# Performance work log

Measured on AMD Instinct MI355X. Metric: run time of the kernel, lower is better.

The kernel has to match this reference:

```python
import jax, jax.numpy as jnp
import numpy as np

B, T, I, H, HOUT = 512, 256, 32, 128, 1
H2 = H // 2


def setup_inputs() -> dict:
    key = jax.random.key(0)
    ks = jax.random.split(key, 16)
    s = lambda *shape: 1.0 / np.sqrt(H)
    def u(k, shape):
        return jax.random.uniform(k, shape, jnp.float32, -1.0 / np.sqrt(H), 1.0 / np.sqrt(H))
    return {
        "x": jax.random.normal(ks[0], (B, T, I), jnp.float32),
        # layer 0 LSTM weights (PyTorch layout: [4H, in], gate order i,f,g,o)
        "w_ih0": u(ks[1], (4 * H, I)),
        "w_hh0": u(ks[2], (4 * H, H)),
        "b_ih0": u(ks[3], (4 * H,)),
        "b_hh0": u(ks[4], (4 * H,)),
        # layer 1 LSTM weights
        "w_ih1": u(ks[5], (4 * H, H)),
        "w_hh1": u(ks[6], (4 * H, H)),
        "b_ih1": u(ks[7], (4 * H,)),
        "b_hh1": u(ks[8], (4 * H,)),
        # MLP head: Linear(H, H//2) -> ReLU -> Linear(H//2, HOUT)
        "fc1_w": u(ks[9], (H2, H)),
        "fc1_b": u(ks[10], (H2,)),
        "fc2_w": u(ks[11], (HOUT, H2)),
        "fc2_b": u(ks[12], (HOUT,)),
    }


def _lstm_layer(x, w_ih, w_hh, b_ih, b_hh):
    # x: (B, T, in) -> h sequence (B, T, H). Dropout is eval-mode identity.
    b, t, _ = x.shape
    h_dim = w_hh.shape[1]
    # precompute input-to-gate projections for the whole sequence (one big GEMM)
    xg = jnp.einsum("bti,gi->btg", x, w_ih) + b_ih + b_hh  # (B, T, 4H)
    xg = jnp.swapaxes(xg, 0, 1)  # (T, B, 4H) for scan

    def step(carry, g_t):
        h, c = carry
        gates = g_t + h @ w_hh.T  # (B, 4H)
        i, f, g, o = jnp.split(gates, 4, axis=-1)  # PyTorch gate order i,f,g,o
        i = jax.nn.sigmoid(i)
        f = jax.nn.sigmoid(f)
        g = jnp.tanh(g)
        o = jax.nn.sigmoid(o)
        c_new = f * c + i * g
        h_new = o * jnp.tanh(c_new)
        return (h_new, c_new), h_new

    zeros = jnp.zeros((b, h_dim), x.dtype)
    _, hs = jax.lax.scan(step, (zeros, zeros), xg)
    return jnp.swapaxes(hs, 0, 1)  # (B, T, H)


def reference(x, w_ih0, w_hh0, b_ih0, b_hh0, w_ih1, w_hh1, b_ih1, b_hh1,
              fc1_w, fc1_b, fc2_w, fc2_b):
    h0 = _lstm_layer(x, w_ih0, w_hh0, b_ih0, b_hh0)   # (B, T, H)
    h1 = _lstm_layer(h0, w_ih1, w_hh1, b_ih1, b_hh1)  # (B, T, H)
    last = h1[:, -1, :]  # (B, H); dropout = identity in eval
    z = jax.nn.relu(last @ fc1_w.T + fc1_b)  # (B, H//2)
    return z @ fc2_w.T + fc2_b  # (B, forecast_horizon)
```

## Files before the change

### kernel.cpp

```cpp
#include <hip/hip_runtime.h>

#define NB 512
#define NT 256
#define NI 32
#define NH 128
#define NG 512
#define WIN 4
#define NWIN 64
#define RING 16
#define NWRK 192

#define L2E  1.4426950408889634f
#define L2E2 2.8853900817779268f

typedef __attribute__((ext_vector_type(8))) short bf16x8;
typedef __attribute__((ext_vector_type(4))) float f32x4;

__device__ __forceinline__ unsigned short f2bf_rne(float f) {
    unsigned u = __float_as_uint(f);
    return (unsigned short)((u + 0x7FFFu + ((u >> 16) & 1u)) >> 16);
}
__device__ __forceinline__ void split2(float a, float b, unsigned& hi, unsigned& lo) {
    unsigned short ha = f2bf_rne(a), hb = f2bf_rne(b);
    float ra = a - __uint_as_float((unsigned)ha << 16);
    float rb = b - __uint_as_float((unsigned)hb << 16);
    hi = (unsigned)ha | ((unsigned)hb << 16);
    lo = (unsigned)f2bf_rne(ra) | ((unsigned)f2bf_rne(rb) << 16);
}
__device__ __forceinline__ bf16x8 u4bf(uint4 u) {
    union { uint4 u; bf16x8 v; } c; c.u = u; return c.v;
}
#define MFMA16(accv, av, bv) \
    accv = __builtin_amdgcn_mfma_f32_16x16x32_bf16(av, bv, accv, 0, 0, 0)

__device__ __forceinline__ void lds_barrier() {
    asm volatile("s_waitcnt lgkmcnt(0)\n\ts_barrier" ::: "memory");
}
__device__ __forceinline__ void vm_drain() {
    asm volatile("s_waitcnt vmcnt(0)" ::: "memory");
}

__device__ __forceinline__ unsigned long long ald64(const unsigned long long* p) {
    return __hip_atomic_load(p, __ATOMIC_RELAXED, __HIP_MEMORY_SCOPE_AGENT);
}
__device__ __forceinline__ void ast64(unsigned long long* p, unsigned long long v) {
    __hip_atomic_store(p, v, __ATOMIC_RELAXED, __HIP_MEMORY_SCOPE_AGENT);
}
__device__ __forceinline__ unsigned aldu(const unsigned* p) {
    return __hip_atomic_load(p, __ATOMIC_RELAXED, __HIP_MEMORY_SCOPE_AGENT);
}
__device__ __forceinline__ void astu(unsigned* p, unsigned v) {
    __hip_atomic_store(p, v, __ATOMIC_RELAXED, __HIP_MEMORY_SCOPE_AGENT);
}

__device__ __forceinline__ float activ(float mi, float mf, float mg, float mo,
                                       float& c) {
    float ei = exp2f(mi), ef = exp2f(mf), eg = exp2f(mg), eo = exp2f(mo);
    float rf  = __builtin_amdgcn_rcpf(1.0f + ef);
    float rig = __builtin_amdgcn_rcpf((1.0f + ei) * (1.0f + eg));
    float cn  = c * rf + (1.0f - eg) * rig;
    c = cn;
    float ec = exp2f(cn * -L2E2);
    float rh = __builtin_amdgcn_rcpf((1.0f + eo) * (1.0f + ec));
    return (1.0f - ec) * rh;
}

__global__ __launch_bounds__(512, 1)
void fused(const float* __restrict__ x,
           const float* __restrict__ w_hh0, const float* __restrict__ w_hh1,
           const float* __restrict__ w_ih0, const float* __restrict__ b_ih0,
           const float* __restrict__ b_hh0,
           const float* __restrict__ w_ih1, const float* __restrict__ b_ih1,
           const float* __restrict__ b_hh1,
           const float* __restrict__ fc1w, const float* __restrict__ fc1b,
           const float* __restrict__ fc2w, const float* __restrict__ fc2b,
           unsigned long long* __restrict__ h0pl,
           float* __restrict__ xgr,
           float* __restrict__ h1s, float* __restrict__ out,
           unsigned* __restrict__ ctr0, unsigned* __restrict__ flagW,
           unsigned* __restrict__ ctr1)
{
    __shared__ __align__(16) unsigned short HA[2][16][128];
    __shared__ __align__(16) unsigned short HL[2][16][128];

    const int bid  = blockIdx.x;
    const int tid  = threadIdx.x;
    const int wv   = tid >> 6;
    const int lane = tid & 63;
    const int quad = lane >> 4;
    const int ml   = lane & 15;

    if (bid >= 64) {
        const int wk = bid - 64;
        for (int tile = wk; tile < 32 * NWIN; tile += NWRK) {
            const int w  = tile >> 5;
            const int pp = tile & 31;
            while (aldu(&ctr0[pp * 16]) < (unsigned)(4 * w + 4))
                __builtin_amdgcn_s_sleep(8);
            if (w >= RING)
                while (aldu(&ctr1[pp * 16]) < (unsigned)(w - (RING - 1)))
                    __builtin_amdgcn_s_sleep(8);
            asm volatile("" ::: "memory");

            bf16x8 A[4][4][2];
#pragma unroll
            for (int tt = 0; tt < 4; ++tt)
#pragma unroll
                for (int q = 0; q < 4; ++q)
#pragma unroll
                    for (int pl = 0; pl < 2; ++pl) {
                        const unsigned long long* ap =
                            h0pl + (((size_t)(4 * w + tt) * 2 + pl) * 32 + pp) * 512
                                 + ml * 32 + q * 8 + quad * 2;
                        unsigned long long a0 = ald64(ap), a1 = ald64(ap + 1);
                        uint4 U;
                        U.x = (unsigned)a0; U.y = (unsigned)(a0 >> 32);
                        U.z = (unsigned)a1; U.w = (unsigned)(a1 >> 32);
                        A[tt][q][pl] = u4bf(U);
                    }

            f32x4 acc[4][4] = {};
#pragma unroll
            for (int nt = 0; nt < 4; ++nt) {
                const float* bw = w_ih1
                    + (size_t)(wv * 64 + nt * 16 + ml) * NH + quad * 8;
                bf16x8 bh[4], bl[4];
#pragma unroll
                for (int q = 0; q < 4; ++q) {
                    float4 v0 = *(const float4*)(bw + q * 32);
                    float4 v1 = *(const float4*)(bw + q * 32 + 4);
                    uint4 H, L;
                    split2(v0.x, v0.y, H.x, L.x); split2(v0.z, v0.w, H.y, L.y);
                    split2(v1.x, v1.y, H.z, L.z); split2(v1.z, v1.w, H.w, L.w);
                    bh[q] = u4bf(H); bl[q] = u4bf(L);
                }
#pragma unroll
                for (int tt = 0; tt < 4; ++tt)
#pragma unroll
                    for (int q = 0; q < 4; ++q) {
                        MFMA16(acc[tt][nt], A[tt][q][0], bh[q]);
                        MFMA16(acc[tt][nt], A[tt][q][1], bh[q]);
                        MFMA16(acc[tt][nt], A[tt][q][0], bl[q]);
                    }
            }

            const int slot = w & (RING - 1);
            float* cb = xgr + ((size_t)slot * 32 + pp) * WIN * 8192;
#pragma unroll
            for (int nt = 0; nt < 4; ++nt) {
                int n = wv * 64 + nt * 16 + ml;
                float s = ((n >> 7) == 2) ? L2E2 : L2E;
                float nbs = -(b_ih1[n] + b_hh1[n]) * s;
#pragma unroll
                for (int tt = 0; tt < 4; ++tt) {
                    float* cp = cb + (size_t)tt * 8192 + n * 16 + quad * 4;
                    float v0 = fmaf(acc[tt][nt][0], -s, nbs);
                    float v1 = fmaf(acc[tt][nt][1], -s, nbs);
                    float v2 = fmaf(acc[tt][nt][2], -s, nbs);
                    float v3 = fmaf(acc[tt][nt][3], -s, nbs);
                    ast64((unsigned long long*)cp,
                          (unsigned long long)__float_as_uint(v0) |
                          ((unsigned long long)__float_as_uint(v1) << 32));
                    ast64((unsigned long long*)(cp + 2),
                          (unsigned long long)__float_as_uint(v2) |
                          ((unsigned long long)__float_as_uint(v3) << 32));
                }
            }
            vm_drain();
            __syncthreads();
            if (tid == 0) astu(&flagW[pp * 64 + w], 1u);
        }
        return;
    }

    const int role = bid >> 5;
    const int p    = bid & 31;
    const int j    = 16 * wv + ml;
    const float* wsrc = role ? w_hh1 : w_hh0;

    bf16x8 wh[4][4], wl[4][4];
#pragma unroll
    for (int t = 0; t < 4; ++t) {
        const float sc = (t == 2) ? L2E2 : L2E;
#pragma unroll
        for (int q = 0; q < 4; ++q) {
            int n = (t * 8 + wv) * 16 + ml;
            const float* s = wsrc + (size_t)n * NH + q * 32 + quad * 8;
            float4 v0 = *(const float4*)s;
            float4 v1 = *(const float4*)(s + 4);
            uint4 H, L;
            split2(v0.x * sc, v0.y * sc, H.x, L.x); split2(v0.z * sc, v0.w * sc, H.y, L.y);
            split2(v1.x * sc, v1.y * sc, H.z, L.z); split2(v1.z * sc, v1.w * sc, H.w, L.w);
            wh[t][q] = u4bf(H);
            wl[t][q] = u4bf(L);
        }
    }

    int ro[4];
#pragma unroll
    for (int q = 0; q < 4; ++q)
        ro[q] = ((ml * 256 + q * 64 + quad * 16) ^ ((ml & 7) << 4));
    int wo[4];
#pragma unroll
    for (int r = 0; r < 4; ++r) {
        int m = quad * 4 + r;
        wo[r] = ((m * 256 + j * 2) ^ ((m & 7) << 4));
    }

    float cr[4] = {};
#pragma unroll
    for (int r = 0; r < 4; ++r) {
        *(unsigned short*)((char*)&HA[0][0][0] + wo[r]) = 0;
        *(unsigned short*)((char*)&HL[0][0][0] + wo[r]) = 0;
    }
    __syncthreads();

    if (role == 0) {
        bf16x8 wi_h[4], wi_l[4];
        float nb[4];
#pragma unroll
        for (int t = 0; t < 4; ++t) {
            const float sc = (t == 2) ? L2E2 : L2E;
            int n = (t * 8 + wv) * 16 + ml;
            const float* s = w_ih0 + (size_t)n * NI + quad * 8;
            float4 v0 = *(const float4*)s;
            float4 v1 = *(const float4*)(s + 4);
            uint4 H, L;
            split2(v0.x * sc, v0.y * sc, H.x, L.x); split2(v0.z * sc, v0.w * sc, H.y, L.y);
            split2(v1.x * sc, v1.y * sc, H.z, L.z); split2(v1.z * sc, v1.w * sc, H.w, L.w);
            wi_h[t] = u4bf(H);
            wi_l[t] = u4bf(L);
            int nn = t * 128 + j;
            nb[t] = -(b_ih0[nn] + b_hh0[nn]) * sc;
        }

        const int erow = tid >> 5;
        const int eoff = erow * 256 + (((tid & 31) * 8) ^ ((erow & 7) << 4));

        const float* xrow = x + (size_t)(p * 16 + ml) * NT * NI + quad * 8;
        auto xload = [&](float4& a, float4& b, int T) __attribute__((always_inline)) {
            const float* sp = xrow + (size_t)T * NI;
            a = *(const float4*)sp;
            b = *(const float4*)(sp + 4);
        };

        auto exp0 = [&](int T, int BUF) __attribute__((always_inline)) {
            unsigned long long vh =
                *(const unsigned long long*)((const char*)&HA[BUF][0][0] + eoff);
            unsigned long long vl =
                *(const unsigned long long*)((const char*)&HL[BUF][0][0] + eoff);
            ast64(h0pl + (((size_t)(T - 1) * 2 + 0) * 32 + p) * 512 + tid, vh);
            ast64(h0pl + (((size_t)(T - 1) * 2 + 1) * 32 + p) * 512 + tid, vl);
        };

        auto step0 = [&](int TL, int BUF, float4 x0, float4 x1)
            __attribute__((always_inline)) {
            const char* hb = (const char*)&HA[BUF][0][0];
            const char* lb = (const char*)&HL[BUF][0][0];
            char* hbn = (char*)&HA[BUF ^ 1][0][0];
            char* lbn = (char*)&HL[BUF ^ 1][0][0];
            uint4 XH, XL;
            split2(x0.x, x0.y, XH.x, XL.x); split2(x0.z, x0.w, XH.y, XL.y);
            split2(x1.x, x1.y, XH.z, XL.z); split2(x1.z, x1.w, XH.w, XL.w);
            bf16x8 xh = u4bf(XH), xl = u4bf(XL);
            f32x4 P[4] = {}, Q[4] = {};
#pragma unroll
            for (int t = 0; t < 4; ++t) {
                MFMA16(P[t], xh, wi_h[t]);
                MFMA16(Q[t], xl, wi_h[t]);
                MFMA16(Q[t], xh, wi_l[t]);
            }
#pragma unroll
            for (int q = 0; q < 4; ++q) {
                bf16x8 ah = *(const bf16x8*)(hb + ro[q]);
                bf16x8 al = *(const bf16x8*)(lb + ro[q]);
#pragma unroll
                for (int t = 0; t < 4; ++t) {
                    MFMA16(P[t], ah, wh[t][q]);
                    MFMA16(Q[t], al, wh[t][q]);
                    if (q & 1) { MFMA16(P[t], ah, wl[t][q]); }
                    else       { MFMA16(Q[t], ah, wl[t][q]); }
                }
            }
#pragma unroll
            for (int r = 0; r < 4; ++r) {
                float mi = nb[0] - P[0][r] - Q[0][r];
                float mf = nb[1] - P[1][r] - Q[1][r];
                float mg = nb[2] - P[2][r] - Q[2][r];
                float mo = nb[3] - P[3][r] - Q[3][r];
                float hn = activ(mi, mf, mg, mo, cr[r]);
                unsigned short hi = f2bf_rne(hn);
                float res = hn - __uint_as_float((unsigned)hi << 16);
                unsigned short lo = f2bf_rne(res);
                *(unsigned short*)(hbn + wo[r]) = hi;
                *(unsigned short*)(lbn + wo[r]) = lo;
            }
        };

        float4 xa0, xa1, xb0, xb1;
        xload(xa0, xa1, 0);
        for (int t = 0; t < 256; t += 2) {
            if (t > 0) {
                exp0(t, 0);
                if ((t & 3) == 0) {
                    vm_drain();
                    __syncthreads();
                    if (tid == 0) astu(&ctr0[p * 16], (unsigned)t);
                }
            }
            xload(xb0, xb1, t + 1);
            step0(t, 0, xa0, xa1);
            lds_barrier();
            exp0(t + 1, 1);
            xload(xa0, xa1, t + 2 > 255 ? 255 : t + 2);
            step0(t + 1, 1, xb0, xb1);
            lds_barrier();
        }
        exp0(256, 0);
        vm_drain();
        __syncthreads();
        if (tid == 0) astu(&ctr0[p * 16], 256u);
        return;
    }

    {
        auto pxg = [&](float (&d)[4][4], int u) __attribute__((always_inline)) {
            int slot = (u >> 2) & (RING - 1);
            int tt   = u & 3;
            const float* b = xgr + (((size_t)slot * 32 + p) * WIN + tt) * 8192
                                 + j * 16 + quad * 4;
#pragma unroll
            for (int tg = 0; tg < 4; ++tg) {
                unsigned long long a0 = ald64((const unsigned long long*)(b + tg * 2048));
                unsigned long long a1 = ald64((const unsigned long long*)(b + tg * 2048 + 2));
                d[tg][0] = __uint_as_float((unsigned)a0);
                d[tg][1] = __uint_as_float((unsigned)(a0 >> 32));
                d[tg][2] = __uint_as_float((unsigned)a1);
                d[tg][3] = __uint_as_float((unsigned)(a1 >> 32));
            }
        };

        auto step1 = [&](int TL, int BUF, const float (&xgv)[4][4])
            __attribute__((always_inline)) {
            const char* hb = (const char*)&HA[BUF][0][0];
            const char* lb = (const char*)&HL[BUF][0][0];
            char* hbn = (char*)&HA[BUF ^ 1][0][0];
            char* lbn = (char*)&HL[BUF ^ 1][0][0];
            f32x4 P[4] = {}, Q[4] = {};
#pragma unroll
            for (int q = 0; q < 4; ++q) {
                bf16x8 ah = *(const bf16x8*)(hb + ro[q]);
                bf16x8 al = *(const bf16x8*)(lb + ro[q]);
#pragma unroll
                for (int t = 0; t < 4; ++t) {
                    MFMA16(P[t], ah, wh[t][q]);
                    MFMA16(Q[t], al, wh[t][q]);
                    if (q & 1) { MFMA16(P[t], ah, wl[t][q]); }
                    else       { MFMA16(Q[t], ah, wl[t][q]); }
                }
            }
#pragma unroll
            for (int r = 0; r < 4; ++r) {
                float mi = xgv[0][r] - P[0][r] - Q[0][r];
                float mf = xgv[1][r] - P[1][r] - Q[1][r];
                float mg = xgv[2][r] - P[2][r] - Q[2][r];
                float mo = xgv[3][r] - P[3][r] - Q[3][r];
                float hn = activ(mi, mf, mg, mo, cr[r]);
                unsigned short hi = f2bf_rne(hn);
                float res = hn - __uint_as_float((unsigned)hi << 16);
                unsigned short lo = f2bf_rne(res);
                *(unsigned short*)(hbn + wo[r]) = hi;
                *(unsigned short*)(lbn + wo[r]) = lo;
                if (TL == 255)
                    h1s[(size_t)(p * 16 + quad * 4 + r) * NH + j] = hn;
            }
        };

        while (aldu(&flagW[p * 64 + 0]) == 0) __builtin_amdgcn_s_sleep(8);
        asm volatile("" ::: "memory");
        float xga[4][4], xgb[4][4];
        pxg(xga, 0);

        for (int u = 0; u < 256; u += 2) {
            if ((u & 3) == 0 && u > 0) {
                if (tid == 0) astu(&ctr1[p * 16], (unsigned)(u >> 2));
            }
            if ((u & 3) == 2 && (u >> 2) < NWIN - 1) {
                int wn = (u >> 2) + 1;
                while (aldu(&flagW[p * 64 + wn]) == 0) __builtin_amdgcn_s_sleep(8);
                asm volatile("" ::: "memory");
            }
            pxg(xgb, u + 1 > 255 ? 255 : u + 1);
            step1(u, 0, xga);
            lds_barrier();
            pxg(xga, u + 2 > 255 ? 255 : u + 2);
            step1(u + 1, 1, xgb);
            lds_barrier();
        }

        vm_drain();
        __syncthreads();
        const int g = tid >> 5;
        const int l = tid & 31;
        const float4* h4 = (const float4*)(h1s + (size_t)(p * 16 + g) * NH);
        const float4* w0 = (const float4*)(fc1w + (size_t)l * NH);
        const float4* w1 = (const float4*)(fc1w + (size_t)(l + 32) * NH);
        float a0 = fc1b[l], a1 = fc1b[l + 32];
#pragma unroll
        for (int q = 0; q < 32; ++q) {
            float4 h = h4[q], u = w0[q], v = w1[q];
            a0 += u.x * h.x + u.y * h.y + u.z * h.z + u.w * h.w;
            a1 += v.x * h.x + v.y * h.y + v.z * h.z + v.w * h.w;
        }
        float pv = fc2w[l] * fmaxf(a0, 0.f) + fc2w[l + 32] * fmaxf(a1, 0.f);
#pragma unroll
        for (int off = 16; off > 0; off >>= 1) pv += __shfl_down(pv, off, 32);
        if (l == 0) out[p * 16 + g] = pv + fc2b[0];
    }
}

extern "C" void kernel_launch(void* const* d_in, const int* in_sizes, int n_in,
                              void* d_out, int out_size, void* d_ws, size_t ws_size,
                              hipStream_t stream)
{
    const float* x     = (const float*)d_in[0];
    const float* w_ih0 = (const float*)d_in[1];
    const float* w_hh0 = (const float*)d_in[2];
    const float* b_ih0 = (const float*)d_in[3];
    const float* b_hh0 = (const float*)d_in[4];
    const float* w_ih1 = (const float*)d_in[5];
    const float* w_hh1 = (const float*)d_in[6];
    const float* b_ih1 = (const float*)d_in[7];
    const float* b_hh1 = (const float*)d_in[8];
    const float* fc1w  = (const float*)d_in[9];
    const float* fc1b  = (const float*)d_in[10];
    const float* fc2w  = (const float*)d_in[11];
    const float* fc2b  = (const float*)d_in[12];
    float* out = (float*)d_out;
    float* ws  = (float*)d_ws;

    size_t o_h0  = 0;
    size_t o_xgr = o_h0 + (size_t)256 * 2 * 32 * 1024;
    size_t o_h1s = o_xgr + (size_t)RING * 32 * WIN * 8192;
    size_t o_flg = o_h1s + (size_t)NB * NH;

    unsigned long long* h0pl = (unsigned long long*)(ws + o_h0);
    float*    xgr   = ws + o_xgr;
    float*    h1sp  = ws + o_h1s;
    unsigned* ctr0  = (unsigned*)(ws + o_flg);
    unsigned* flagW = ctr0 + 32 * 16;
    unsigned* ctr1  = flagW + 32 * 64;

    hipMemsetAsync(ctr0, 0, (32 * 16 + 32 * 64 + 32 * 16) * sizeof(unsigned),
                   stream);

    void* args[] = {
        (void*)&x,
        (void*)&w_hh0, (void*)&w_hh1,
        (void*)&w_ih0, (void*)&b_ih0, (void*)&b_hh0,
        (void*)&w_ih1, (void*)&b_ih1, (void*)&b_hh1,
        (void*)&fc1w, (void*)&fc1b, (void*)&fc2w, (void*)&fc2b,
        (void*)&h0pl, (void*)&xgr, (void*)&h1sp, (void*)&out,
        (void*)&ctr0, (void*)&flagW, (void*)&ctr1,
    };
    hipLaunchCooperativeKernel((const void*)fused, dim3(256), dim3(512),
                               args, 0, stream);
}
```

Baseline: 739.9 us.

## Fuse layer-1 input projection into recurrent blocks, drop worker blocks

Removes the 192 worker blocks that computed layer-1 input-gate projections into a global ring buffer. Layer-1 recurrent blocks now keep W_ih1 as split-bf16 registers and run the projection per step with MFMA, reading layer-0 h from global into double-buffered LDS. This drops the xg ring traffic and the flag handshakes, and the grid shrinks to 64 blocks. In exchange each layer-1 step on the serial critical path carries extra MFMA work, register pressure rises, and staging h0 through LDS adds a dependency.

After: 2.813 ms. 280% more time.

```diff
diff --git a/kernel.cpp b/kernel.cpp
--- a/kernel.cpp
+++ b/kernel.cpp
@@ -5,16 +5,13 @@
 #define NI 32
 #define NH 128
 #define NG 512
-#define WIN 4
-#define NWIN 64
-#define RING 16
-#define NWRK 192
 
 #define L2E  1.4426950408889634f
 #define L2E2 2.8853900817779268f
 
 typedef __attribute__((ext_vector_type(8))) short bf16x8;
 typedef __attribute__((ext_vector_type(4))) float f32x4;
+typedef unsigned long long u64;
 
 __device__ __forceinline__ unsigned short f2bf_rne(float f) {
     unsigned u = __float_as_uint(f);
@@ -40,10 +37,10 @@
     asm volatile("s_waitcnt vmcnt(0)" ::: "memory");
 }
 
-__device__ __forceinline__ unsigned long long ald64(const unsigned long long* p) {
+__device__ __forceinline__ u64 ald64(const u64* p) {
     return __hip_atomic_load(p, __ATOMIC_RELAXED, __HIP_MEMORY_SCOPE_AGENT);
 }
-__device__ __forceinline__ void ast64(unsigned long long* p, unsigned long long v) {
+__device__ __forceinline__ void ast64(u64* p, u64 v) {
     __hip_atomic_store(p, v, __ATOMIC_RELAXED, __HIP_MEMORY_SCOPE_AGENT);
 }
 __device__ __forceinline__ unsigned aldu(const unsigned* p) {
@@ -74,14 +71,14 @@
            const float* __restrict__ b_hh1,
            const float* __restrict__ fc1w, const float* __restrict__ fc1b,
            const float* __restrict__ fc2w, const float* __restrict__ fc2b,
-           unsigned long long* __restrict__ h0pl,
-           float* __restrict__ xgr,
+           u64* __restrict__ h0pl,
            float* __restrict__ h1s, float* __restrict__ out,
-           unsigned* __restrict__ ctr0, unsigned* __restrict__ flagW,
-           unsigned* __restrict__ ctr1)
+           unsigned* __restrict__ ctr0)
 {
     __shared__ __align__(16) unsigned short HA[2][16][128];
     __shared__ __align__(16) unsigned short HL[2][16][128];
+    __shared__ __align__(16) unsigned short GH[2][16][128];
+    __shared__ __align__(16) unsigned short GL[2][16][128];
 
     const int bid  = blockIdx.x;
     const int tid  = threadIdx.x;
@@ -89,90 +86,6 @@
     const int lane = tid & 63;
     const int quad = lane >> 4;
     const int ml   = lane & 15;
-
-    if (bid >= 64) {
-        const int wk = bid - 64;
-        for (int tile = wk; tile < 32 * NWIN; tile += NWRK) {
-            const int w  = tile >> 5;
-            const int pp = tile & 31;
-            while (aldu(&ctr0[pp * 16]) < (unsigned)(4 * w + 4))
-                __builtin_amdgcn_s_sleep(8);
-            if (w >= RING)
-                while (aldu(&ctr1[pp * 16]) < (unsigned)(w - (RING - 1)))
-                    __builtin_amdgcn_s_sleep(8);
-            asm volatile("" ::: "memory");
-
-            bf16x8 A[4][4][2];
-#pragma unroll
-            for (int tt = 0; tt < 4; ++tt)
-#pragma unroll
-                for (int q = 0; q < 4; ++q)
-#pragma unroll
-                    for (int pl = 0; pl < 2; ++pl) {
-                        const unsigned long long* ap =
-                            h0pl + (((size_t)(4 * w + tt) * 2 + pl) * 32 + pp) * 512
-                                 + ml * 32 + q * 8 + quad * 2;
-                        unsigned long long a0 = ald64(ap), a1 = ald64(ap + 1);
-                        uint4 U;
-                        U.x = (unsigned)a0; U.y = (unsigned)(a0 >> 32);
-                        U.z = (unsigned)a1; U.w = (unsigned)(a1 >> 32);
-                        A[tt][q][pl] = u4bf(U);
-                    }
-
-            f32x4 acc[4][4] = {};
-#pragma unroll
-            for (int nt = 0; nt < 4; ++nt) {
-                const float* bw = w_ih1
-                    + (size_t)(wv * 64 + nt * 16 + ml) * NH + quad * 8;
-                bf16x8 bh[4], bl[4];
-#pragma unroll
-                for (int q = 0; q < 4; ++q) {
-                    float4 v0 = *(const float4*)(bw + q * 32);
-                    float4 v1 = *(const float4*)(bw + q * 32 + 4);
-                    uint4 H, L;
-                    split2(v0.x, v0.y, H.x, L.x); split2(v0.z, v0.w, H.y, L.y);
-                    split2(v1.x, v1.y, H.z, L.z); split2(v1.z, v1.w, H.w, L.w);
-                    bh[q] = u4bf(H); bl[q] = u4bf(L);
-                }
-#pragma unroll
-                for (int tt = 0; tt < 4; ++tt)
-#pragma unroll
-                    for (int q = 0; q < 4; ++q) {
-                        MFMA16(acc[tt][nt], A[tt][q][0], bh[q]);
-                        MFMA16(acc[tt][nt], A[tt][q][1], bh[q]);
-                        MFMA16(acc[tt][nt], A[tt][q][0], bl[q]);
-                    }
-            }
-
-            const int slot = w & (RING - 1);
-            float* cb = xgr + ((size_t)slot * 32 + pp) * WIN * 8192;
-#pragma unroll
-            for (int nt = 0; nt < 4; ++nt) {
-                int n = wv * 64 + nt * 16 + ml;
-                float s = ((n >> 7) == 2) ? L2E2 : L2E;
-                float nbs = -(b_ih1[n] + b_hh1[n]) * s;
-#pragma unroll
-                for (int tt = 0; tt < 4; ++tt) {
-                    float* cp = cb + (size_t)tt * 8192 + n * 16 + quad * 4;
-                    float v0 = fmaf(acc[tt][nt][0], -s, nbs);
-                    float v1 = fmaf(acc[tt][nt][1], -s, nbs);
-                    float v2 = fmaf(acc[tt][nt][2], -s, nbs);
-                    float v3 = fmaf(acc[tt][nt][3], -s, nbs);
-                    ast64((unsigned long long*)cp,
-                          (unsigned long long)__float_as_uint(v0) |
-                          ((unsigned long long)__float_as_uint(v1) << 32));
-                    ast64((unsigned long long*)(cp + 2),
-                          (unsigned long long)__float_as_uint(v2) |
-                          ((unsigned long long)__float_as_uint(v3) << 32));
-                }
-            }
-            vm_drain();
-            __syncthreads();
-            if (tid == 0) astu(&flagW[pp * 64 + w], 1u);
-        }
-        return;
-    }
-
     const int role = bid >> 5;
     const int p    = bid & 31;
     const int j    = 16 * wv + ml;
@@ -245,10 +158,8 @@
         };
 
         auto exp0 = [&](int T, int BUF) __attribute__((always_inline)) {
-            unsigned long long vh =
-                *(const unsigned long long*)((const char*)&HA[BUF][0][0] + eoff);
-            unsigned long long vl =
-                *(const unsigned long long*)((const char*)&HL[BUF][0][0] + eoff);
+            u64 vh = *(const u64*)((const char*)&HA[BUF][0][0] + eoff);
+            u64 vl = *(const u64*)((const char*)&HL[BUF][0][0] + eoff);
             ast64(h0pl + (((size_t)(T - 1) * 2 + 0) * 32 + p) * 512 + tid, vh);
             ast64(h0pl + (((size_t)(T - 1) * 2 + 1) * 32 + p) * 512 + tid, vl);
         };
@@ -324,29 +235,68 @@
     }
 
     {
-        auto pxg = [&](float (&d)[4][4], int u) __attribute__((always_inline)) {
-            int slot = (u >> 2) & (RING - 1);
-            int tt   = u & 3;
-            const float* b = xgr + (((size_t)slot * 32 + p) * WIN + tt) * 8192
-                                 + j * 16 + quad * 4;
-#pragma unroll
-            for (int tg = 0; tg < 4; ++tg) {
-                unsigned long long a0 = ald64((const unsigned long long*)(b + tg * 2048));
-                unsigned long long a1 = ald64((const unsigned long long*)(b + tg * 2048 + 2));
-                d[tg][0] = __uint_as_float((unsigned)a0);
-                d[tg][1] = __uint_as_float((unsigned)(a0 >> 32));
-                d[tg][2] = __uint_as_float((unsigned)a1);
-                d[tg][3] = __uint_as_float((unsigned)(a1 >> 32));
-            }
-        };
-
-        auto step1 = [&](int TL, int BUF, const float (&xgv)[4][4])
-            __attribute__((always_inline)) {
+        bf16x8 vih[4][4], vil[4][4];
+        float nb[4];
+#pragma unroll
+        for (int t = 0; t < 4; ++t) {
+            const float sc = (t == 2) ? L2E2 : L2E;
+#pragma unroll
+            for (int q = 0; q < 4; ++q) {
+                int n = (t * 8 + wv) * 16 + ml;
+                const float* s = w_ih1 + (size_t)n * NH + q * 32 + quad * 8;
+                float4 v0 = *(const float4*)s;
+                float4 v1 = *(const float4*)(s + 4);
+                uint4 H, L;
+                split2(v0.x * sc, v0.y * sc, H.x, L.x); split2(v0.z * sc, v0.w * sc, H.y, L.y);
+                split2(v1.x * sc, v1.y * sc, H.z, L.z); split2(v1.z * sc, v1.w * sc, H.w, L.w);
+                vih[t][q] = u4bf(H);
+                vil[t][q] = u4bf(L);
+            }
+            int nn = t * 128 + j;
+            nb[t] = -(b_ih1[nn] + b_hh1[nn]) * sc;
+        }
+
+        const int gm = tid >> 5;
+        const int go = gm * 256 + (((tid & 31) * 8) ^ ((gm & 7) << 4));
+
+        auto pld = [&](u64& a, u64& b, int T) __attribute__((always_inline)) {
+            int Tc = T < 255 ? T : 255;
+            a = ald64(h0pl + (((size_t)Tc * 2 + 0) * 32 + p) * 512 + tid);
+            b = ald64(h0pl + (((size_t)Tc * 2 + 1) * 32 + p) * 512 + tid);
+        };
+        auto gwr = [&](u64 a, u64 b, int BUF) __attribute__((always_inline)) {
+            *(u64*)((char*)&GH[BUF][0][0] + go) = a;
+            *(u64*)((char*)&GL[BUF][0][0] + go) = b;
+        };
+        auto wwait = [&](int need) __attribute__((always_inline)) {
+            if (tid == 0) {
+                while ((int)aldu(&ctr0[p * 16]) < need)
+                    __builtin_amdgcn_s_sleep(4);
+            }
+            __syncthreads();
+            asm volatile("" ::: "memory");
+        };
+
+        auto step1 = [&](int TL, int BUF) __attribute__((always_inline)) {
             const char* hb = (const char*)&HA[BUF][0][0];
             const char* lb = (const char*)&HL[BUF][0][0];
+            const char* gb = (const char*)&GH[BUF][0][0];
+            const char* glb = (const char*)&GL[BUF][0][0];
             char* hbn = (char*)&HA[BUF ^ 1][0][0];
             char* lbn = (char*)&HL[BUF ^ 1][0][0];
             f32x4 P[4] = {}, Q[4] = {};
+#pragma unroll
+            for (int q = 0; q < 4; ++q) {
+                bf16x8 gh = *(const bf16x8*)(gb + ro[q]);
+                bf16x8 gl = *(const bf16x8*)(glb + ro[q]);
+#pragma unroll
+                for (int t = 0; t < 4; ++t) {
+                    MFMA16(P[t], gh, vih[t][q]);
+                    MFMA16(Q[t], gl, vih[t][q]);
+                    if (q & 1) { MFMA16(P[t], gh, vil[t][q]); }
+                    else       { MFMA16(Q[t], gh, vil[t][q]); }
+                }
+            }
 #pragma unroll
             for (int q = 0; q < 4; ++q) {
                 bf16x8 ah = *(const bf16x8*)(hb + ro[q]);
@@ -361,10 +311,10 @@
             }
 #pragma unroll
             for (int r = 0; r < 4; ++r) {
-                float mi = xgv[0][r] - P[0][r] - Q[0][r];
-                float mf = xgv[1][r] - P[1][r] - Q[1][r];
-                float mg = xgv[2][r] - P[2][r] - Q[2][r];
-                float mo = xgv[3][r] - P[3][r] - Q[3][r];
+                float mi = nb[0] - P[0][r] - Q[0][r];
+                float mf = nb[1] - P[1][r] - Q[1][r];
+                float mg = nb[2] - P[2][r] - Q[2][r];
+                float mo = nb[3] - P[3][r] - Q[3][r];
                 float hn = activ(mi, mf, mg, mo, cr[r]);
                 unsigned short hi = f2bf_rne(hn);
                 float res = hn - __uint_as_float((unsigned)hi << 16);
@@ -376,25 +326,22 @@
             }
         };
 
-        while (aldu(&flagW[p * 64 + 0]) == 0) __builtin_amdgcn_s_sleep(8);
-        asm volatile("" ::: "memory");
-        float xga[4][4], xgb[4][4];
-        pxg(xga, 0);
-
-        for (int u = 0; u < 256; u += 2) {
-            if ((u & 3) == 0 && u > 0) {
-                if (tid == 0) astu(&ctr1[p * 16], (unsigned)(u >> 2));
-            }
-            if ((u & 3) == 2 && (u >> 2) < NWIN - 1) {
-                int wn = (u >> 2) + 1;
-                while (aldu(&flagW[p * 64 + wn]) == 0) __builtin_amdgcn_s_sleep(8);
-                asm volatile("" ::: "memory");
-            }
-            pxg(xgb, u + 1 > 255 ? 255 : u + 1);
-            step1(u, 0, xga);
+        wwait(4);
+        u64 a0, a1, b0, b1;
+        pld(a0, a1, 0);
+        gwr(a0, a1, 0);
+        pld(b0, b1, 1);
+        __syncthreads();
+
+        for (int t = 0; t < 256; t += 2) {
+            if ((t & 3) == 2) wwait(t + 6 > 256 ? 256 : t + 6);
+            gwr(b0, b1, 1);
+            pld(a0, a1, t + 2);
+            step1(t, 0);
             lds_barrier();
-            pxg(xga, u + 2 > 255 ? 255 : u + 2);
-            step1(u + 1, 1, xgb);
+            gwr(a0, a1, 0);
+            pld(b0, b1, t + 3);
+            step1(t + 1, 1);
             lds_barrier();
         }
 
@@ -405,14 +352,14 @@
         const float4* h4 = (const float4*)(h1s + (size_t)(p * 16 + g) * NH);
         const float4* w0 = (const float4*)(fc1w + (size_t)l * NH);
         const float4* w1 = (const float4*)(fc1w + (size_t)(l + 32) * NH);
-        float a0 = fc1b[l], a1 = fc1b[l + 32];
+        float a0f = fc1b[l], a1f = fc1b[l + 32];
 #pragma unroll
         for (int q = 0; q < 32; ++q) {
             float4 h = h4[q], u = w0[q], v = w1[q];
-            a0 += u.x * h.x + u.y * h.y + u.z * h.z + u.w * h.w;
-            a1 += v.x * h.x + v.y * h.y + v.z * h.z + v.w * h.w;
-        }
-        float pv = fc2w[l] * fmaxf(a0, 0.f) + fc2w[l + 32] * fmaxf(a1, 0.f);
+            a0f += u.x * h.x + u.y * h.y + u.z * h.z + u.w * h.w;
+            a1f += v.x * h.x + v.y * h.y + v.z * h.z + v.w * h.w;
+        }
+        float pv = fc2w[l] * fmaxf(a0f, 0.f) + fc2w[l + 32] * fmaxf(a1f, 0.f);
 #pragma unroll
         for (int off = 16; off > 0; off >>= 1) pv += __shfl_down(pv, off, 32);
         if (l == 0) out[p * 16 + g] = pv + fc2b[0];
@@ -440,19 +387,14 @@
     float* ws  = (float*)d_ws;
 
     size_t o_h0  = 0;
-    size_t o_xgr = o_h0 + (size_t)256 * 2 * 32 * 1024;
-    size_t o_h1s = o_xgr + (size_t)RING * 32 * WIN * 8192;
-    size_t o_flg = o_h1s + (size_t)NB * NH;
-
-    unsigned long long* h0pl = (unsigned long long*)(ws + o_h0);
-    float*    xgr   = ws + o_xgr;
-    float*    h1sp  = ws + o_h1s;
-    unsigned* ctr0  = (unsigned*)(ws + o_flg);
-    unsigned* flagW = ctr0 + 32 * 16;
-    unsigned* ctr1  = flagW + 32 * 64;
-
-    hipMemsetAsync(ctr0, 0, (32 * 16 + 32 * 64 + 32 * 16) * sizeof(unsigned),
-                   stream);
+    size_t o_h1s = o_h0 + (size_t)256 * 2 * 32 * 1024;
+    size_t o_ctr = o_h1s + (size_t)NB * NH;
+
+    u64*      h0pl = (u64*)(ws + o_h0);
+    float*    h1sp = ws + o_h1s;
+    unsigned* ctr0 = (unsigned*)(ws + o_ctr);
+
+    hipMemsetAsync(ctr0, 0, 32 * 16 * sizeof(unsigned), stream);
 
     void* args[] = {
         (void*)&x,
@@ -460,9 +402,8 @@
         (void*)&w_ih0, (void*)&b_ih0, (void*)&b_hh0,
         (void*)&w_ih1, (void*)&b_ih1, (void*)&b_hh1,
         (void*)&fc1w, (void*)&fc1b, (void*)&fc2w, (void*)&fc2b,
-        (void*)&h0pl, (void*)&xgr, (void*)&h1sp, (void*)&out,
-        (void*)&ctr0, (void*)&flagW, (void*)&ctr1,
+        (void*)&h0pl, (void*)&h1sp, (void*)&out, (void*)&ctr0,
     };
-    hipLaunchCooperativeKernel((const void*)fused, dim3(256), dim3(512),
+    hipLaunchCooperativeKernel((const void*)fused, dim3(64), dim3(512),
                                args, 0, stream);
 }
```

## Relayout xg ring buffer, deepen layer-1 prefetch, single-thread flag wait

Applied to the files above, without the earlier changes.

Changes the layout of the precomputed layer-1 input-gate ring buffer so that the consumer's loads from a quad are contiguous in j instead of strided by 16. The layer-1 recurrence loop is unrolled by four with four register buffers, so xg loads are prefetched two steps ahead instead of one. The flag spin-wait moves to thread 0 followed by a block barrier, with a shorter sleep. This adds register pressure and an extra __syncthreads per window.

Result: no change. 729.1 us (-1.5%).

```diff
diff --git a/kernel.cpp b/kernel.cpp
--- a/kernel.cpp
+++ b/kernel.cpp
@@ -15,6 +15,7 @@
 
 typedef __attribute__((ext_vector_type(8))) short bf16x8;
 typedef __attribute__((ext_vector_type(4))) float f32x4;
+typedef unsigned long long u64;
 
 __device__ __forceinline__ unsigned short f2bf_rne(float f) {
     unsigned u = __float_as_uint(f);
@@ -40,10 +41,10 @@
     asm volatile("s_waitcnt vmcnt(0)" ::: "memory");
 }
 
-__device__ __forceinline__ unsigned long long ald64(const unsigned long long* p) {
+__device__ __forceinline__ u64 ald64(const u64* p) {
     return __hip_atomic_load(p, __ATOMIC_RELAXED, __HIP_MEMORY_SCOPE_AGENT);
 }
-__device__ __forceinline__ void ast64(unsigned long long* p, unsigned long long v) {
+__device__ __forceinline__ void ast64(u64* p, u64 v) {
     __hip_atomic_store(p, v, __ATOMIC_RELAXED, __HIP_MEMORY_SCOPE_AGENT);
 }
 __device__ __forceinline__ unsigned aldu(const unsigned* p) {
@@ -74,7 +75,7 @@
            const float* __restrict__ b_hh1,
            const float* __restrict__ fc1w, const float* __restrict__ fc1b,
            const float* __restrict__ fc2w, const float* __restrict__ fc2b,
-           unsigned long long* __restrict__ h0pl,
+           u64* __restrict__ h0pl,
            float* __restrict__ xgr,
            float* __restrict__ h1s, float* __restrict__ out,
            unsigned* __restrict__ ctr0, unsigned* __restrict__ flagW,
@@ -109,10 +110,10 @@
                 for (int q = 0; q < 4; ++q)
 #pragma unroll
                     for (int pl = 0; pl < 2; ++pl) {
-                        const unsigned long long* ap =
+                        const u64* ap =
                             h0pl + (((size_t)(4 * w + tt) * 2 + pl) * 32 + pp) * 512
                                  + ml * 32 + q * 8 + quad * 2;
-                        unsigned long long a0 = ald64(ap), a1 = ald64(ap + 1);
+                        u64 a0 = ald64(ap), a1 = ald64(ap + 1);
                         uint4 U;
                         U.x = (unsigned)a0; U.y = (unsigned)(a0 >> 32);
                         U.z = (unsigned)a1; U.w = (unsigned)(a1 >> 32);
@@ -151,19 +152,20 @@
                 int n = wv * 64 + nt * 16 + ml;
                 float s = ((n >> 7) == 2) ? L2E2 : L2E;
                 float nbs = -(b_ih1[n] + b_hh1[n]) * s;
+                int aoff = quad * 2048 + (n >> 7) * 512 + (n & 127) * 4;
 #pragma unroll
                 for (int tt = 0; tt < 4; ++tt) {
-                    float* cp = cb + (size_t)tt * 8192 + n * 16 + quad * 4;
+                    float* cp = cb + (size_t)tt * 8192 + aoff;
                     float v0 = fmaf(acc[tt][nt][0], -s, nbs);
                     float v1 = fmaf(acc[tt][nt][1], -s, nbs);
                     float v2 = fmaf(acc[tt][nt][2], -s, nbs);
                     float v3 = fmaf(acc[tt][nt][3], -s, nbs);
-                    ast64((unsigned long long*)cp,
-                          (unsigned long long)__float_as_uint(v0) |
-                          ((unsigned long long)__float_as_uint(v1) << 32));
-                    ast64((unsigned long long*)(cp + 2),
-                          (unsigned long long)__float_as_uint(v2) |
-                          ((unsigned long long)__float_as_uint(v3) << 32));
+                    ast64((u64*)cp,
+                          (u64)__float_as_uint(v0) |
+                          ((u64)__float_as_uint(v1) << 32));
+                    ast64((u64*)(cp + 2),
+                          (u64)__float_as_uint(v2) |
+                          ((u64)__float_as_uint(v3) << 32));
                 }
             }
             vm_drain();
@@ -245,10 +247,8 @@
         };
 
         auto exp0 = [&](int T, int BUF) __attribute__((always_inline)) {
-            unsigned long long vh =
-                *(const unsigned long long*)((const char*)&HA[BUF][0][0] + eoff);
-            unsigned long long vl =
-                *(const unsigned long long*)((const char*)&HL[BUF][0][0] + eoff);
+            u64 vh = *(const u64*)((const char*)&HA[BUF][0][0] + eoff);
+            u64 vl = *(const u64*)((const char*)&HL[BUF][0][0] + eoff);
             ast64(h0pl + (((size_t)(T - 1) * 2 + 0) * 32 + p) * 512 + tid, vh);
             ast64(h0pl + (((size_t)(T - 1) * 2 + 1) * 32 + p) * 512 + tid, vl);
         };
@@ -325,14 +325,15 @@
 
     {
         auto pxg = [&](float (&d)[4][4], int u) __attribute__((always_inline)) {
-            int slot = (u >> 2) & (RING - 1);
-            int tt   = u & 3;
+            int uc = u < 255 ? u : 255;
+            int slot = (uc >> 2) & (RING - 1);
+            int tt   = uc & 3;
             const float* b = xgr + (((size_t)slot * 32 + p) * WIN + tt) * 8192
-                                 + j * 16 + quad * 4;
+                                 + quad * 2048 + j * 4;
 #pragma unroll
             for (int tg = 0; tg < 4; ++tg) {
-                unsigned long long a0 = ald64((const unsigned long long*)(b + tg * 2048));
-                unsigned long long a1 = ald64((const unsigned long long*)(b + tg * 2048 + 2));
+                u64 a0 = ald64((const u64*)(b + tg * 512));
+                u64 a1 = ald64((const u64*)(b + tg * 512 + 2));
                 d[tg][0] = __uint_as_float((unsigned)a0);
                 d[tg][1] = __uint_as_float((unsigned)(a0 >> 32));
                 d[tg][2] = __uint_as_float((unsigned)a1);
@@ -376,25 +377,34 @@
             }
         };
 
-        while (aldu(&flagW[p * 64 + 0]) == 0) __builtin_amdgcn_s_sleep(8);
-        asm volatile("" ::: "memory");
-        float xga[4][4], xgb[4][4];
-        pxg(xga, 0);
-
-        for (int u = 0; u < 256; u += 2) {
-            if ((u & 3) == 0 && u > 0) {
-                if (tid == 0) astu(&ctr1[p * 16], (unsigned)(u >> 2));
-            }
-            if ((u & 3) == 2 && (u >> 2) < NWIN - 1) {
-                int wn = (u >> 2) + 1;
-                while (aldu(&flagW[p * 64 + wn]) == 0) __builtin_amdgcn_s_sleep(8);
-                asm volatile("" ::: "memory");
-            }
-            pxg(xgb, u + 1 > 255 ? 255 : u + 1);
-            step1(u, 0, xga);
-            lds_barrier();
-            pxg(xga, u + 2 > 255 ? 255 : u + 2);
-            step1(u + 1, 1, xgb);
+        auto waitflag = [&](int wn) __attribute__((always_inline)) {
+            if (tid == 0) {
+                while (aldu(&flagW[p * 64 + wn]) == 0)
+                    __builtin_amdgcn_s_sleep(2);
+            }
+            __syncthreads();
+            asm volatile("" ::: "memory");
+        };
+
+        waitflag(0);
+        float xa[4][4], xb[4][4], xc[4][4], xd[4][4];
+        pxg(xa, 0);
+        pxg(xb, 1);
+
+        for (int u = 0; u < 256; u += 4) {
+            if (u > 0 && tid == 0) astu(&ctr1[p * 16], (unsigned)(u >> 2));
+            pxg(xc, u + 2);
+            step1(u, 0, xa);
+            lds_barrier();
+            pxg(xd, u + 3);
+            step1(u + 1, 1, xb);
+            lds_barrier();
+            if (u + 4 < 256) waitflag((u + 4) >> 2);
+            pxg(xa, u + 4);
+            step1(u + 2, 0, xc);
+            lds_barrier();
+            pxg(xb, u + 5);
+            step1(u + 3, 1, xd);
             lds_barrier();
         }
 
@@ -444,10 +454,10 @@
     size_t o_h1s = o_xgr + (size_t)RING * 32 * WIN * 8192;
     size_t o_flg = o_h1s + (size_t)NB * NH;
 
-    unsigned long long* h0pl = (unsigned long long*)(ws + o_h0);
-    float*    xgr   = ws + o_xgr;
-    float*    h1sp  = ws + o_h1s;
-    unsigned* ctr0  = (unsigned*)(ws + o_flg);
+    u64*      h0pl = (u64*)(ws + o_h0);
+    float*    xgr  = ws + o_xgr;
+    float*    h1sp = ws + o_h1s;
+    unsigned* ctr0 = (unsigned*)(ws + o_flg);
     unsigned* flagW = ctr0 + 32 * 16;
     unsigned* ctr1  = flagW + 32 * 64;
 
```
